# Performance work log

Measured on AMD Instinct MI355X. Metric: run time of the kernel, lower is better.

The kernel has to match this reference:

```python
import jax, jax.numpy as jnp
import numpy as np

N = 1024
D = 64

def setup_inputs() -> dict:
    key = jax.random.key(0)
    ks = jax.random.split(key, 8)
    s = lambda k, shp, fan: jax.random.normal(k, shp, dtype=jnp.float32) * (1.0 / np.sqrt(fan))
    return {
        "cell_states": jax.random.normal(ks[0], (N, D), dtype=jnp.float32),
        "adjacency": jax.random.uniform(ks[1], (N, N), dtype=jnp.float32) * 0.1,
        "gate_w1": s(ks[2], (64, 2 * D), 2 * D),
        "gate_b1": jnp.zeros((64,), jnp.float32),
        "gate_w2": s(ks[3], (32, 64), 64),
        "gate_b2": jnp.zeros((32,), jnp.float32),
        "gate_w3": s(ks[4], (1, 32), 32),
        "gate_b3": jnp.zeros((1,), jnp.float32),
        "sig_w": s(ks[5], (D, D), D),
        "sig_b": jnp.zeros((D,), jnp.float32),
    }

def reference(cell_states, adjacency, gate_w1, gate_b1, gate_w2, gate_b2,
              gate_w3, gate_b3, sig_w, sig_b):
    n = cell_states.shape[0]
    eye = jnp.eye(n, dtype=cell_states.dtype)
    # symmetrize, zero diagonal, row-softmax (diagonal zeros still participate in softmax)
    sym_adj = 0.5 * (adjacency + adjacency.T) * (1.0 - eye)
    norm_adj = jax.nn.softmax(sym_adj, axis=1)  # [N, N]
    # gate MLP on concat(x_i, x_j): split first linear to avoid materializing [N,N,2D]
    w1a, w1b = gate_w1[:, :D], gate_w1[:, D:]
    hi = cell_states @ w1a.T          # [N, 64] contribution of own state i
    hj = cell_states @ w1b.T          # [N, 64] contribution of other state j
    h1 = jax.nn.relu(hi[:, None, :] + hj[None, :, :] + gate_b1)   # [N, N, 64]
    h2 = jax.nn.relu(jnp.einsum('ijk,hk->ijh', h1, gate_w2) + gate_b2)  # [N, N, 32]
    gate = jax.nn.sigmoid(jnp.einsum('ijh,oh->ijo', h2, gate_w3) + gate_b3)[..., 0]  # [N, N]
    transferred = cell_states @ sig_w.T + sig_b   # [N, D]
    # exclude i == j pairs (loop skips them)
    weight = gate * norm_adj * (1.0 - eye)        # [N, N]
    return cell_states + weight @ transferred     # [N, D]
```

## Files before the change

kernel.cpp:

```cpp
#include <hip/hip_runtime.h>
#include <hip/hip_bf16.h>

#define N 1024
#define D 64

typedef __attribute__((ext_vector_type(8))) short bf16x8;
typedef __attribute__((ext_vector_type(16))) float f32x16;

__device__ __forceinline__ short f2bf(float x) {
    __hip_bfloat16 b = __float2bfloat16(x);
    return __builtin_bit_cast(short, b);
}

__global__ __launch_bounds__(256) void symS_kernel(
    const float* __restrict__ A, float* __restrict__ S,
    float* __restrict__ maxp, float* __restrict__ sump)
{
    __shared__ float t2[64 * 65];
    const int bi = blockIdx.x, bj = blockIdx.y;
    const int t = threadIdx.x;
    #pragma unroll
    for (int k = 0; k < 4; k++) {
        int f4 = t + 256 * k;
        int r2 = f4 >> 4, c4 = (f4 & 15) * 4;
        float4 v = *(const float4*)&A[(size_t)(bj * 64 + r2) * N + bi * 64 + c4];
        t2[r2 * 65 + c4 + 0] = v.x;
        t2[r2 * 65 + c4 + 1] = v.y;
        t2[r2 * 65 + c4 + 2] = v.z;
        t2[r2 * 65 + c4 + 3] = v.w;
    }
    __syncthreads();
    const int r  = t >> 2;
    const int cq = (t & 3) * 16;
    const int gi = bi * 64 + r;
    float vals[16];
    #pragma unroll
    for (int k = 0; k < 4; k++) {
        float4 a1 = *(const float4*)&A[(size_t)gi * N + bj * 64 + cq + k * 4];
        float tmp[4] = {a1.x, a1.y, a1.z, a1.w};
        #pragma unroll
        for (int e = 0; e < 4; e++) {
            int c = cq + k * 4 + e;
            float sv = 0.5f * (tmp[e] + t2[c * 65 + r]);
            if (bi == bj && r == c) sv = 0.0f;
            vals[k * 4 + e] = sv;
        }
    }
    #pragma unroll
    for (int k = 0; k < 4; k++) {
        float4 sv = {vals[k * 4], vals[k * 4 + 1], vals[k * 4 + 2], vals[k * 4 + 3]};
        *(float4*)&S[(size_t)gi * N + bj * 64 + cq + k * 4] = sv;
    }
    float mx = vals[0];
    #pragma unroll
    for (int e = 1; e < 16; e++) mx = fmaxf(mx, vals[e]);
    mx = fmaxf(mx, __shfl_xor(mx, 1));
    mx = fmaxf(mx, __shfl_xor(mx, 2));
    float s = 0.0f;
    #pragma unroll
    for (int e = 0; e < 16; e++) s += __expf(vals[e] - mx);
    s += __shfl_xor(s, 1);
    s += __shfl_xor(s, 2);
    if ((t & 3) == 0) {
        maxp[(size_t)gi * 16 + bj] = mx;
        sump[(size_t)gi * 16 + bj] = s;
    }
}

__global__ __launch_bounds__(256) void stats2_kernel(
    const float* __restrict__ maxp, const float* __restrict__ sump,
    float* __restrict__ m_ws, float* __restrict__ rs_ws)
{
    const int row = blockIdx.x * 256 + threadIdx.x;
    float m = -1e30f;
    #pragma unroll
    for (int k = 0; k < 16; k++) m = fmaxf(m, maxp[(size_t)row * 16 + k]);
    float s = 0.0f;
    #pragma unroll
    for (int k = 0; k < 16; k++)
        s += sump[(size_t)row * 16 + k] * __expf(maxp[(size_t)row * 16 + k] - m);
    m_ws[row]  = m;
    rs_ws[row] = 1.0f / s;
}

__global__ __launch_bounds__(256) void precompute_kernel(
    const float* __restrict__ cell, const float* __restrict__ w1,
    const float* __restrict__ b1, const float* __restrict__ sw,
    const float* __restrict__ sb,
    float* __restrict__ hi, float* __restrict__ hjb, float* __restrict__ trf)
{
    __shared__ float w1s[64 * 129];
    __shared__ float sws[64 * 65];
    __shared__ float xs[4 * 64];
    const int t = threadIdx.x;
    const int b = blockIdx.x;
    #pragma unroll
    for (int k = 0; k < 8; k++) {
        int f4 = t + 256 * k;
        int row = f4 >> 5, c4 = (f4 & 31) * 4;
        float4 v = *(const float4*)&w1[(size_t)row * 128 + c4];
        w1s[row * 129 + c4 + 0] = v.x;
        w1s[row * 129 + c4 + 1] = v.y;
        w1s[row * 129 + c4 + 2] = v.z;
        w1s[row * 129 + c4 + 3] = v.w;
    }
    #pragma unroll
    for (int k = 0; k < 4; k++) {
        int f4 = t + 256 * k;
        int row = f4 >> 4, c4 = (f4 & 15) * 4;
        float4 v = *(const float4*)&sw[(size_t)row * 64 + c4];
        sws[row * 65 + c4 + 0] = v.x;
        sws[row * 65 + c4 + 1] = v.y;
        sws[row * 65 + c4 + 2] = v.z;
        sws[row * 65 + c4 + 3] = v.w;
    }
    xs[t] = cell[(size_t)b * 256 + t];
    __syncthreads();
    const int wv = t >> 6, l = t & 63;
    const float* xr = &xs[wv * 64];
    float a0 = 0.0f, a1 = 0.0f, a2 = 0.0f;
    #pragma unroll 16
    for (int d = 0; d < 64; d++) {
        float x = xr[d];
        a0 = fmaf(x, w1s[l * 129 + d], a0);
        a1 = fmaf(x, w1s[l * 129 + 64 + d], a1);
        a2 = fmaf(x, sws[l * 65 + d], a2);
    }
    const int i = b * 4 + wv;
    hi[(size_t)i * D + l]  = a0;
    hjb[(size_t)i * D + l] = a1 + b1[l];
    trf[(size_t)i * D + l] = a2 + sb[l];
}

__global__ __launch_bounds__(256, 3) void gate_fused_kernel(
    const float* __restrict__ S, const float* __restrict__ hi,
    const float* __restrict__ hjb, const float* __restrict__ trf,
    const float* __restrict__ w2, const float* __restrict__ b2,
    const float* __restrict__ w3, const float* __restrict__ b3,
    const float* __restrict__ m_ws, const float* __restrict__ rs_ws,
    float* __restrict__ part)
{
    __shared__ float smem[8192];
    float* hjb_s = smem;
    float* S_s   = smem + 4096;
    const int t   = threadIdx.x;
    const int w   = t >> 6;
    const int l   = t & 63;
    const int i0  = blockIdx.x * 32;
    const int by  = blockIdx.y;
    const int jb0 = by * 64;
    const int jbase = jb0 + w * 16;
    const int p   = l & 31;
    const int hi8 = l >> 5;
    const int i_mine = i0 + p;

    #pragma unroll
    for (int k = 0; k < 4; k++) {
        int f4 = t + 256 * k;
        float4 v = *(const float4*)&hjb[(size_t)jb0 * D + f4 * 4];
        *(float4*)&hjb_s[f4 * 4] = v;
    }
    #pragma unroll
    for (int k = 0; k < 2; k++) {
        int f4 = t + 256 * k;
        int row = f4 >> 3, c4 = (f4 & 7) * 4;
        float4 v = *(const float4*)&S[(size_t)(jb0 + row) * N + i0 + c4];
        *(float4*)&S_s[row * 32 + c4] = v;
    }

    float hv[32];
    #pragma unroll
    for (int q = 0; q < 4; q++) {
        float4 v0 = *(const float4*)&hi[(size_t)i_mine * D + q * 16 + hi8 * 8];
        float4 v1 = *(const float4*)&hi[(size_t)i_mine * D + q * 16 + hi8 * 8 + 4];
        hv[q * 8 + 0] = v0.x; hv[q * 8 + 1] = v0.y;
        hv[q * 8 + 2] = v0.z; hv[q * 8 + 3] = v0.w;
        hv[q * 8 + 4] = v1.x; hv[q * 8 + 5] = v1.y;
        hv[q * 8 + 6] = v1.z; hv[q * 8 + 7] = v1.w;
    }
    bf16x8 wa[4];
    #pragma unroll
    for (int q = 0; q < 4; q++) {
        const float* wp = &w2[(size_t)p * D + q * 16 + hi8 * 8];
        #pragma unroll
        for (int e = 0; e < 8; e++) wa[q][e] = f2bf(wp[e]);
    }
    float b2r[16], w3r[16];
    #pragma unroll
    for (int r = 0; r < 16; r++) {
        int ch = (r & 3) + 8 * (r >> 2) + 4 * hi8;
        b2r[r] = b2[ch];
        w3r[r] = w3[ch];
    }
    const float m_mine  = m_ws[i_mine];
    const float rs_mine = rs_ws[i_mine];
    const float b3v     = b3[0];

    __syncthreads();

    bf16x8 wf = {0, 0, 0, 0, 0, 0, 0, 0};
    #pragma unroll
    for (int jj = 0; jj < 16; jj++) {
        const int j_loc = w * 16 + jj;
        const int j = jb0 + j_loc;
        bf16x8 bq[4];
        #pragma unroll
        for (int q = 0; q < 4; q++) {
            float4 h0 = *(const float4*)&hjb_s[j_loc * 64 + q * 16 + hi8 * 8];
            float4 h1 = *(const float4*)&hjb_s[j_loc * 64 + q * 16 + hi8 * 8 + 4];
            bq[q][0] = f2bf(fmaxf(hv[q * 8 + 0] + h0.x, 0.0f));
            bq[q][1] = f2bf(fmaxf(hv[q * 8 + 1] + h0.y, 0.0f));
            bq[q][2] = f2bf(fmaxf(hv[q * 8 + 2] + h0.z, 0.0f));
            bq[q][3] = f2bf(fmaxf(hv[q * 8 + 3] + h0.w, 0.0f));
            bq[q][4] = f2bf(fmaxf(hv[q * 8 + 4] + h1.x, 0.0f));
            bq[q][5] = f2bf(fmaxf(hv[q * 8 + 5] + h1.y, 0.0f));
            bq[q][6] = f2bf(fmaxf(hv[q * 8 + 6] + h1.z, 0.0f));
            bq[q][7] = f2bf(fmaxf(hv[q * 8 + 7] + h1.w, 0.0f));
        }
        f32x16 accA, accB;
        #pragma unroll
        for (int r = 0; r < 16; r++) { accA[r] = b2r[r]; accB[r] = 0.0f; }
        accA = __builtin_amdgcn_mfma_f32_32x32x16_bf16(wa[0], bq[0], accA, 0, 0, 0);
        accA = __builtin_amdgcn_mfma_f32_32x32x16_bf16(wa[1], bq[1], accA, 0, 0, 0);
        accB = __builtin_amdgcn_mfma_f32_32x32x16_bf16(wa[2], bq[2], accB, 0, 0, 0);
        accB = __builtin_amdgcn_mfma_f32_32x32x16_bf16(wa[3], bq[3], accB, 0, 0, 0);

        float gp = 0.0f;
        #pragma unroll
        for (int r = 0; r < 16; r++)
            gp = fmaf(fmaxf(accA[r] + accB[r], 0.0f), w3r[r], gp);
        gp += __shfl_xor(gp, 32);

        float gate = 1.0f / (1.0f + __expf(-(gp + b3v)));
        float sym  = S_s[j_loc * 32 + p];
        float wgt  = (i_mine == j) ? 0.0f
                                   : gate * __expf(sym - m_mine) * rs_mine;
        short wb = f2bf(wgt);
        wf[jj & 7] = ((jj >> 3) == hi8) ? wb : wf[jj & 7];
    }

    bf16x8 tf0, tf1;
    #pragma unroll
    for (int e = 0; e < 8; e++) {
        const float* tp = &trf[(size_t)(jbase + hi8 * 8 + e) * D];
        tf0[e] = f2bf(tp[p]);
        tf1[e] = f2bf(tp[32 + p]);
    }
    f32x16 oA, oB;
    #pragma unroll
    for (int r = 0; r < 16; r++) { oA[r] = 0.0f; oB[r] = 0.0f; }
    oA = __builtin_amdgcn_mfma_f32_32x32x16_bf16(wf, tf0, oA, 0, 0, 0);
    oB = __builtin_amdgcn_mfma_f32_32x32x16_bf16(wf, tf1, oB, 0, 0, 0);

    __syncthreads();
    float* red = smem;
    #pragma unroll
    for (int r = 0; r < 16; r++) {
        int row = (r & 3) + 8 * (r >> 2) + 4 * hi8;
        red[w * 2048 + row * 64 + p]      = oA[r];
        red[w * 2048 + row * 64 + 32 + p] = oB[r];
    }
    __syncthreads();
    #pragma unroll
    for (int e = 0; e < 8; e++) {
        int idx = t + e * 256;
        float s = red[idx] + red[2048 + idx] + red[4096 + idx] + red[6144 + idx];
        part[(size_t)by * (N * D) + (size_t)i0 * D + idx] = s;
    }
}

__global__ __launch_bounds__(256) void reduce_kernel(
    const float* __restrict__ cell, const float* __restrict__ part,
    float* __restrict__ out)
{
    const int idx = blockIdx.x * 256 + threadIdx.x;
    float s = cell[idx];
    #pragma unroll
    for (int k = 0; k < 16; k++) s += part[(size_t)k * (N * D) + idx];
    out[idx] = s;
}

extern "C" void kernel_launch(void* const* d_in, const int* in_sizes, int n_in,
                              void* d_out, int out_size, void* d_ws, size_t ws_size,
                              hipStream_t stream) {
    const float* cell = (const float*)d_in[0];
    const float* adj  = (const float*)d_in[1];
    const float* w1   = (const float*)d_in[2];
    const float* b1   = (const float*)d_in[3];
    const float* w2   = (const float*)d_in[4];
    const float* b2   = (const float*)d_in[5];
    const float* w3   = (const float*)d_in[6];
    const float* b3   = (const float*)d_in[7];
    const float* sw   = (const float*)d_in[8];
    const float* sb   = (const float*)d_in[9];
    float* out = (float*)d_out;

    float* ws    = (float*)d_ws;
    float* m_ws  = ws;
    float* rs_ws = ws + 1024;
    float* hi    = ws + 2048;
    float* hjb   = hi + N * D;
    float* trf   = hjb + N * D;
    float* S     = trf + N * D;
    float* part  = S + (size_t)N * N;
    float* maxp  = part + (size_t)N * D * 16;
    float* sump  = maxp + N * 16;

    symS_kernel<<<dim3(16, 16), 256, 0, stream>>>(adj, S, maxp, sump);
    stats2_kernel<<<4, 256, 0, stream>>>(maxp, sump, m_ws, rs_ws);
    precompute_kernel<<<256, 256, 0, stream>>>(cell, w1, b1, sw, sb, hi, hjb, trf);
    gate_fused_kernel<<<dim3(32, 16), 256, 0, stream>>>(S, hi, hjb, trf,
                                                        w2, b2, w3, b3,
                                                        m_ws, rs_ws, part);
    reduce_kernel<<<256, 256, 0, stream>>>(cell, part, out);
}
```

Before: 35.70 us.

## Fuse adjacency symmetrization and softmax into gate kernel with deferred normalization

Drops the separate symmetrize and softmax-statistics kernels. The gate kernel now reads the adjacency tile and its transpose directly and computes unnormalized exp weights without max subtraction. It also accumulates per-row partial exp sums, and the final kernel divides the accumulated product by the row sum. This removes two launches and the N×N S write and read, at the cost of relying on small adjacency values so that exp without a max shift does not overflow, plus slightly more shared memory.

```diff
diff --git a/kernel.cpp b/kernel.cpp
--- a/kernel.cpp
+++ b/kernel.cpp
@@ -10,77 +10,6 @@
 __device__ __forceinline__ short f2bf(float x) {
     __hip_bfloat16 b = __float2bfloat16(x);
     return __builtin_bit_cast(short, b);
-}
-
-__global__ __launch_bounds__(256) void symS_kernel(
-    const float* __restrict__ A, float* __restrict__ S,
-    float* __restrict__ maxp, float* __restrict__ sump)
-{
-    __shared__ float t2[64 * 65];
-    const int bi = blockIdx.x, bj = blockIdx.y;
-    const int t = threadIdx.x;
-    #pragma unroll
-    for (int k = 0; k < 4; k++) {
-        int f4 = t + 256 * k;
-        int r2 = f4 >> 4, c4 = (f4 & 15) * 4;
-        float4 v = *(const float4*)&A[(size_t)(bj * 64 + r2) * N + bi * 64 + c4];
-        t2[r2 * 65 + c4 + 0] = v.x;
-        t2[r2 * 65 + c4 + 1] = v.y;
-        t2[r2 * 65 + c4 + 2] = v.z;
-        t2[r2 * 65 + c4 + 3] = v.w;
-    }
-    __syncthreads();
-    const int r  = t >> 2;
-    const int cq = (t & 3) * 16;
-    const int gi = bi * 64 + r;
-    float vals[16];
-    #pragma unroll
-    for (int k = 0; k < 4; k++) {
-        float4 a1 = *(const float4*)&A[(size_t)gi * N + bj * 64 + cq + k * 4];
-        float tmp[4] = {a1.x, a1.y, a1.z, a1.w};
-        #pragma unroll
-        for (int e = 0; e < 4; e++) {
-            int c = cq + k * 4 + e;
-            float sv = 0.5f * (tmp[e] + t2[c * 65 + r]);
-            if (bi == bj && r == c) sv = 0.0f;
-            vals[k * 4 + e] = sv;
-        }
-    }
-    #pragma unroll
-    for (int k = 0; k < 4; k++) {
-        float4 sv = {vals[k * 4], vals[k * 4 + 1], vals[k * 4 + 2], vals[k * 4 + 3]};
-        *(float4*)&S[(size_t)gi * N + bj * 64 + cq + k * 4] = sv;
-    }
-    float mx = vals[0];
-    #pragma unroll
-    for (int e = 1; e < 16; e++) mx = fmaxf(mx, vals[e]);
-    mx = fmaxf(mx, __shfl_xor(mx, 1));
-    mx = fmaxf(mx, __shfl_xor(mx, 2));
-    float s = 0.0f;
-    #pragma unroll
-    for (int e = 0; e < 16; e++) s += __expf(vals[e] - mx);
-    s += __shfl_xor(s, 1);
-    s += __shfl_xor(s, 2);
-    if ((t & 3) == 0) {
-        maxp[(size_t)gi * 16 + bj] = mx;
-        sump[(size_t)gi * 16 + bj] = s;
-    }
-}
-
-__global__ __launch_bounds__(256) void stats2_kernel(
-    const float* __restrict__ maxp, const float* __restrict__ sump,
-    float* __restrict__ m_ws, float* __restrict__ rs_ws)
-{
-    const int row = blockIdx.x * 256 + threadIdx.x;
-    float m = -1e30f;
-    #pragma unroll
-    for (int k = 0; k < 16; k++) m = fmaxf(m, maxp[(size_t)row * 16 + k]);
-    float s = 0.0f;
-    #pragma unroll
-    for (int k = 0; k < 16; k++)
-        s += sump[(size_t)row * 16 + k] * __expf(maxp[(size_t)row * 16 + k] - m);
-    m_ws[row]  = m;
-    rs_ws[row] = 1.0f / s;
 }
 
 __global__ __launch_bounds__(256) void precompute_kernel(
@@ -133,16 +62,16 @@
 }
 
 __global__ __launch_bounds__(256, 3) void gate_fused_kernel(
-    const float* __restrict__ S, const float* __restrict__ hi,
+    const float* __restrict__ A, const float* __restrict__ hi,
     const float* __restrict__ hjb, const float* __restrict__ trf,
     const float* __restrict__ w2, const float* __restrict__ b2,
     const float* __restrict__ w3, const float* __restrict__ b3,
-    const float* __restrict__ m_ws, const float* __restrict__ rs_ws,
-    float* __restrict__ part)
+    float* __restrict__ part, float* __restrict__ rsp)
 {
-    __shared__ float smem[8192];
-    float* hjb_s = smem;
-    float* S_s   = smem + 4096;
+    __shared__ float smem[8352];
+    float* S1    = smem;
+    float* T2    = smem + 2048;
+    float* hjb_s = smem + 4128;
     const int t   = threadIdx.x;
     const int w   = t >> 6;
     const int l   = t & 63;
@@ -157,15 +86,24 @@
     #pragma unroll
     for (int k = 0; k < 4; k++) {
         int f4 = t + 256 * k;
-        float4 v = *(const float4*)&hjb[(size_t)jb0 * D + f4 * 4];
-        *(float4*)&hjb_s[f4 * 4] = v;
+        *(float4*)&hjb_s[f4 * 4] = *(const float4*)&hjb[(size_t)jb0 * D + f4 * 4];
     }
     #pragma unroll
     for (int k = 0; k < 2; k++) {
         int f4 = t + 256 * k;
         int row = f4 >> 3, c4 = (f4 & 7) * 4;
-        float4 v = *(const float4*)&S[(size_t)(jb0 + row) * N + i0 + c4];
-        *(float4*)&S_s[row * 32 + c4] = v;
+        *(float4*)&S1[row * 32 + c4] =
+            *(const float4*)&A[(size_t)(jb0 + row) * N + i0 + c4];
+    }
+    #pragma unroll
+    for (int k = 0; k < 2; k++) {
+        int f4 = t + 256 * k;
+        int r = f4 >> 4, c4 = (f4 & 15) * 4;
+        float4 v = *(const float4*)&A[(size_t)(i0 + r) * N + jb0 + c4];
+        T2[r * 65 + c4 + 0] = v.x;
+        T2[r * 65 + c4 + 1] = v.y;
+        T2[r * 65 + c4 + 2] = v.z;
+        T2[r * 65 + c4 + 3] = v.w;
     }
 
     float hv[32];
@@ -192,22 +130,21 @@
         b2r[r] = b2[ch];
         w3r[r] = w3[ch];
     }
-    const float m_mine  = m_ws[i_mine];
-    const float rs_mine = rs_ws[i_mine];
-    const float b3v     = b3[0];
+    const float b3v = b3[0];
 
     __syncthreads();
 
     bf16x8 wf = {0, 0, 0, 0, 0, 0, 0, 0};
+    float es = 0.0f;
     #pragma unroll
     for (int jj = 0; jj < 16; jj++) {
-        const int j_loc = w * 16 + jj;
-        const int j = jb0 + j_loc;
+        const int jl = w * 16 + jj;
+        const int j  = jb0 + jl;
         bf16x8 bq[4];
         #pragma unroll
         for (int q = 0; q < 4; q++) {
-            float4 h0 = *(const float4*)&hjb_s[j_loc * 64 + q * 16 + hi8 * 8];
-            float4 h1 = *(const float4*)&hjb_s[j_loc * 64 + q * 16 + hi8 * 8 + 4];
+            float4 h0 = *(const float4*)&hjb_s[jl * 64 + q * 16 + hi8 * 8];
+            float4 h1 = *(const float4*)&hjb_s[jl * 64 + q * 16 + hi8 * 8 + 4];
             bq[q][0] = f2bf(fmaxf(hv[q * 8 + 0] + h0.x, 0.0f));
             bq[q][1] = f2bf(fmaxf(hv[q * 8 + 1] + h0.y, 0.0f));
             bq[q][2] = f2bf(fmaxf(hv[q * 8 + 2] + h0.z, 0.0f));
@@ -231,20 +168,23 @@
             gp = fmaf(fmaxf(accA[r] + accB[r], 0.0f), w3r[r], gp);
         gp += __shfl_xor(gp, 32);
 
+        const bool isdiag = (i_mine == j);
+        float sym  = 0.5f * (S1[jl * 32 + p] + T2[p * 65 + jl]);
+        float e    = isdiag ? 1.0f : __expf(sym);
         float gate = 1.0f / (1.0f + __expf(-(gp + b3v)));
-        float sym  = S_s[j_loc * 32 + p];
-        float wgt  = (i_mine == j) ? 0.0f
-                                   : gate * __expf(sym - m_mine) * rs_mine;
-        short wb = f2bf(wgt);
-        wf[jj & 7] = ((jj >> 3) == hi8) ? wb : wf[jj & 7];
-    }
+        float u    = isdiag ? 0.0f : gate * e;
+        if ((jj >> 3) == hi8) es += e;
+        short ub = f2bf(u);
+        wf[jj & 7] = ((jj >> 3) == hi8) ? ub : wf[jj & 7];
+    }
+    es += __shfl_xor(es, 32);
 
     bf16x8 tf0, tf1;
     #pragma unroll
-    for (int e = 0; e < 8; e++) {
-        const float* tp = &trf[(size_t)(jbase + hi8 * 8 + e) * D];
-        tf0[e] = f2bf(tp[p]);
-        tf1[e] = f2bf(tp[32 + p]);
+    for (int e8 = 0; e8 < 8; e8++) {
+        const float* tp = &trf[(size_t)(jbase + hi8 * 8 + e8) * D];
+        tf0[e8] = f2bf(tp[p]);
+        tf1[e8] = f2bf(tp[32 + p]);
     }
     f32x16 oA, oB;
     #pragma unroll
@@ -254,12 +194,14 @@
 
     __syncthreads();
     float* red = smem;
+    float* esb = smem + 8192;
     #pragma unroll
     for (int r = 0; r < 16; r++) {
         int row = (r & 3) + 8 * (r >> 2) + 4 * hi8;
         red[w * 2048 + row * 64 + p]      = oA[r];
         red[w * 2048 + row * 64 + 32 + p] = oB[r];
     }
+    if (hi8 == 0) esb[w * 32 + p] = es;
     __syncthreads();
     #pragma unroll
     for (int e = 0; e < 8; e++) {
@@ -267,17 +209,23 @@
         float s = red[idx] + red[2048 + idx] + red[4096 + idx] + red[6144 + idx];
         part[(size_t)by * (N * D) + (size_t)i0 * D + idx] = s;
     }
-}
-
-__global__ __launch_bounds__(256) void reduce_kernel(
+    if (t < 32)
+        rsp[by * N + i0 + t] = esb[t] + esb[32 + t] + esb[64 + t] + esb[96 + t];
+}
+
+__global__ __launch_bounds__(256) void finish_kernel(
     const float* __restrict__ cell, const float* __restrict__ part,
-    float* __restrict__ out)
+    const float* __restrict__ rsp, float* __restrict__ out)
 {
     const int idx = blockIdx.x * 256 + threadIdx.x;
-    float s = cell[idx];
-    #pragma unroll
-    for (int k = 0; k < 16; k++) s += part[(size_t)k * (N * D) + idx];
-    out[idx] = s;
+    const int i = idx >> 6;
+    float rs = 0.0f;
+    #pragma unroll
+    for (int k = 0; k < 16; k++) rs += rsp[k * N + i];
+    float acc = 0.0f;
+    #pragma unroll
+    for (int k = 0; k < 16; k++) acc += part[(size_t)k * (N * D) + idx];
+    out[idx] = cell[idx] + acc / rs;
 }
 
 extern "C" void kernel_launch(void* const* d_in, const int* in_sizes, int n_in,
@@ -296,21 +244,15 @@
     float* out = (float*)d_out;
 
     float* ws    = (float*)d_ws;
-    float* m_ws  = ws;
-    float* rs_ws = ws + 1024;
-    float* hi    = ws + 2048;
+    float* hi    = ws;
     float* hjb   = hi + N * D;
     float* trf   = hjb + N * D;
-    float* S     = trf + N * D;
-    float* part  = S + (size_t)N * N;
-    float* maxp  = part + (size_t)N * D * 16;
-    float* sump  = maxp + N * 16;
-
-    symS_kernel<<<dim3(16, 16), 256, 0, stream>>>(adj, S, maxp, sump);
-    stats2_kernel<<<4, 256, 0, stream>>>(maxp, sump, m_ws, rs_ws);
+    float* part  = trf + N * D;
+    float* rsp   = part + (size_t)N * D * 16;
+
     precompute_kernel<<<256, 256, 0, stream>>>(cell, w1, b1, sw, sb, hi, hjb, trf);
-    gate_fused_kernel<<<dim3(32, 16), 256, 0, stream>>>(S, hi, hjb, trf,
+    gate_fused_kernel<<<dim3(32, 16), 256, 0, stream>>>(adj, hi, hjb, trf,
                                                         w2, b2, w3, b3,
-                                                        m_ws, rs_ws, part);
-    reduce_kernel<<<256, 256, 0, stream>>>(cell, part, out);
-}
+                                                        part, rsp);
+    finish_kernel<<<256, 256, 0, stream>>>(cell, part, rsp, out);
+}
```

Measured after the change: 31.70 us. -11.2%, faster.
